# Performance work log

Measured on AMD Instinct MI355X. Metric: run time of the kernel, lower is better.

The kernel has to match this reference:

```python
import jax, jax.numpy as jnp
import numpy as np

T = 2048; HIDDEN = 2048; HQ = 32; G = 2; D = 64
KERNEL = 32; STRIDE = 16; BLOCK = 64; TOPK = 16
INIT_BLOCKS = 1; LOCAL_BLOCKS = 2; WINDOW = 512
ROPE_BASE = 10000.0
NEG = -1e30


def _rope(x):
    # x: [T, H, D], non-interleaved rotate-half rope
    t, h, d = x.shape
    half = d // 2
    inv = 1.0 / (ROPE_BASE ** (jnp.arange(half, dtype=jnp.float32) / half))
    freqs = jnp.arange(t, dtype=jnp.float32)[:, None] * inv[None, :]
    cos = jnp.cos(freqs)[:, None, :]
    sin = jnp.sin(freqs)[:, None, :]
    x1, x2 = x[..., :half], x[..., half:]
    return jnp.concatenate([x1 * cos - x2 * sin, x2 * cos + x1 * sin], axis=-1)


def setup_inputs() -> dict:
    key = jax.random.key(0)
    ks = jax.random.split(key, 8)
    s = 0.02
    return {
        "hidden_states": jax.random.normal(ks[0], (1, T, HIDDEN), jnp.float32),
        "Wq": jax.random.normal(ks[1], (HQ * D, HIDDEN), jnp.float32) * s,
        "Wk": jax.random.normal(ks[2], (G * D, HIDDEN), jnp.float32) * s,
        "Wv": jax.random.normal(ks[3], (G * D, HIDDEN), jnp.float32) * s,
        "Wo": jax.random.normal(ks[4], (HIDDEN, HQ * D), jnp.float32) * s,
        "Wgate": jax.random.normal(ks[5], (3, HIDDEN), jnp.float32) * s,
        "compress_key": jax.random.normal(ks[6], (G, D * KERNEL, D), jnp.float32) * s,
        "compress_value": jax.random.normal(ks[7], (G, D * KERNEL, D), jnp.float32) * s,
    }


def reference(hidden_states, Wq, Wk, Wv, Wo, Wgate, compress_key, compress_value):
    x = hidden_states[0]                      # [T, HIDDEN] (single varlen sequence)
    scale = 1.0 / np.sqrt(D).astype(np.float32)
    q = (x @ Wq.T).reshape(T, HQ, D)
    k = (x @ Wk.T).reshape(T, G, D)
    v = (x @ Wv.T).reshape(T, G, D)
    gate = jax.nn.sigmoid(x @ Wgate.T)        # [T, 3]
    q = _rope(q)
    k = _rope(k)

    # --- branch 1: compressed attention (linear_compress + compressed_attention) ---
    C = (T - KERNEL) // STRIDE + 1            # compressed sequence length
    starts = jnp.arange(C) * STRIDE
    win_idx = starts[:, None] + jnp.arange(KERNEL)[None, :]        # [C, KERNEL]
    kw = k[win_idx].transpose(2, 0, 1, 3).reshape(G, C, KERNEL * D)
    vw = v[win_idx].transpose(2, 0, 1, 3).reshape(G, C, KERNEL * D)
    ck = jnp.einsum('gcf,gfd->cgd', kw, compress_key)              # [C, G, D]
    cv = jnp.einsum('gcf,gfd->cgd', vw, compress_value)

    qg = q.reshape(T, G, HQ // G, D)          # [T, G, group, D]
    cs = jnp.einsum('tghd,cgd->ghtc', qg, ck) * scale              # [G, grp, T, C]
    # query i may attend compressed token j iff i >= j*stride + kernel - 1
    cmask = jnp.arange(T)[:, None] >= (starts + KERNEL - 1)[None, :]  # [T, C]
    cs = jnp.where(cmask[None, None], cs, NEG)
    p = jax.nn.softmax(cs, axis=-1)
    valid = cmask.any(-1)                     # queries with >=1 compressed key
    p = jnp.where(valid[None, None, :, None], p, 0.0)
    comp_out = jnp.einsum('ghtc,cgd->tghd', p, cv).reshape(T, HQ, D)

    # --- topk block selection from pooled compressed attention scores ---
    NB = T // BLOCK
    bstart = jnp.arange(NB) * BLOCK
    # compressed token j overlaps key block b
    overlap = ((starts[:, None] < bstart[None, :] + BLOCK) &
               (starts[:, None] + KERNEL > bstart[None, :])).astype(p.dtype)  # [C, NB]
    score = jnp.einsum('ghtc,cb->gtb', p, overlap)                 # [G, T, NB]
    qblock = jnp.arange(T) // BLOCK
    b = jnp.arange(NB)
    causal_b = b[None, :] <= qblock[:, None]                       # [T, NB]
    forced = (b[None, :] < INIT_BLOCKS) | (((qblock[:, None] - b[None, :]) < LOCAL_BLOCKS) & causal_b)
    score = jnp.where(forced[None], jnp.inf, score)
    score = jnp.where(causal_b[None], score, -jnp.inf)
    _, topk_idx = jax.lax.top_k(score, TOPK)                       # [G, T, TOPK]
    tk_valid = jnp.take_along_axis(score, topk_idx, axis=-1) > -jnp.inf
    sel = ((topk_idx[..., None] == b) & tk_valid[..., None]).any(axis=2)  # [G, T, NB]

    # --- branch 2: topk block-sparse attention ---
    key_block = jnp.arange(T) // BLOCK
    keymask = sel[:, :, key_block]                                 # [G, T, Tk]
    causal = jnp.arange(T)[:, None] >= jnp.arange(T)[None, :]      # [T, Tk]
    smask = keymask & causal[None]
    ss = jnp.einsum('tghd,sgd->ghts', qg, k) * scale               # [G, grp, T, Tk]
    ss = jnp.where(smask[:, None], ss, NEG)
    sparse_out = jnp.einsum('ghts,sgd->tghd', jax.nn.softmax(ss, -1), v).reshape(T, HQ, D)

    # --- branch 3: sliding window attention (causal, left window) ---
    delta = jnp.arange(T)[:, None] - jnp.arange(T)[None, :]
    wmask = (delta >= 0) & (delta <= WINDOW)                       # [T, Tk]
    ws = jnp.einsum('tghd,sgd->ghts', qg, k) * scale
    ws = jnp.where(wmask[None, None], ws, NEG)
    slide_out = jnp.einsum('ghts,sgd->tghd', jax.nn.softmax(ws, -1), v).reshape(T, HQ, D)

    # --- learned gate fusion + output projection ---
    out = (gate[:, 0, None, None] * comp_out +
           gate[:, 1, None, None] * sparse_out +
           gate[:, 2, None, None] * slide_out)                    # [T, HQ, D]
    o = out.reshape(T, HQ * D) @ Wo.T
    return o[None]                                                 # [1, T, HIDDEN]
```

## Files before the change

kernel.cpp:

```cpp
#include <hip/hip_runtime.h>
#include <math.h>

#define T_SEQ 2048
#define NHQ 32
#define NG 2
#define HD 64
#define CSTRIDE 16
#define KVGW 384

#if defined(__has_builtin)
#if __has_builtin(__builtin_amdgcn_exp2f)
#define EXP2(x) __builtin_amdgcn_exp2f(x)
#endif
#endif
#ifndef EXP2
#define EXP2(x) __expf(0.6931471805599453f * (x))
#endif

typedef __attribute__((ext_vector_type(8))) short short8_t;
typedef __attribute__((ext_vector_type(4))) short short4_t;
typedef __attribute__((ext_vector_type(4))) float f32x4;

__device__ __forceinline__ ushort f2bf(float x) {
  union { float f; unsigned u; } c; c.f = x;
  unsigned r = c.u + 0x7fff + ((c.u >> 16) & 1);
  return (ushort)(r >> 16);
}
__device__ __forceinline__ float bf2f(ushort u) {
  union { unsigned u; float f; } c; c.u = ((unsigned)u) << 16;
  return c.f;
}

__device__ __forceinline__ void glds16(const ushort* g, ushort* l) {
  __builtin_amdgcn_global_load_lds(
      (const __attribute__((address_space(1))) unsigned int*)g,
      (__attribute__((address_space(3))) unsigned int*)l, 16, 0, 0);
}

__global__ __launch_bounds__(256) void mgemm(
    const ushort* __restrict__ A, const ushort* __restrict__ B,
    float* __restrict__ C, int M, int N, int K) {
  __shared__ __align__(16) ushort As[128 * 64];
  __shared__ __align__(16) ushort Bs[64 * 64];
  const int tid = threadIdx.x;
  const int lane = tid & 63, w = tid >> 6;
  const int quad = lane >> 4, l16 = lane & 15;
  const int m0 = blockIdx.y * 128, n0 = blockIdx.x * 64;
  const int mq = (w & 1) * 64, nq = (w >> 1) * 32;
  f32x4 acc[4][2];
  const f32x4 fz = {0.f, 0.f, 0.f, 0.f};
  #pragma unroll
  for (int i = 0; i < 4; ++i)
    #pragma unroll
    for (int j = 0; j < 2; ++j) acc[i][j] = fz;

  for (int k0 = 0; k0 < K; k0 += 64) {
    __syncthreads();
    #pragma unroll
    for (int j = 0; j < 4; ++j) {
      int ci = j * 256 + tid;
      int row = ci >> 3, cl = ci & 7;
      int kc = cl ^ (row & 7);
      glds16(A + ((size_t)(m0 + row) * K + k0 + kc * 8), &As[ci * 8]);
    }
    #pragma unroll
    for (int j = 0; j < 2; ++j) {
      int ci = j * 256 + tid;
      int row = ci >> 3, cl = ci & 7;
      int kc = cl ^ (row & 7);
      glds16(B + ((size_t)(n0 + row) * K + k0 + kc * 8), &Bs[ci * 8]);
    }
    __syncthreads();
    #pragma unroll
    for (int kt = 0; kt < 2; ++kt) {
      short8_t af[4], bf_[2];
      #pragma unroll
      for (int mt = 0; mt < 4; ++mt) {
        int row = mq + mt * 16 + l16;
        int cl = (kt * 4 + quad) ^ (row & 7);
        af[mt] = *(const short8_t*)&As[row * 64 + cl * 8];
      }
      #pragma unroll
      for (int nt = 0; nt < 2; ++nt) {
        int row = nq + nt * 16 + l16;
        int cl = (kt * 4 + quad) ^ (row & 7);
        bf_[nt] = *(const short8_t*)&Bs[row * 64 + cl * 8];
      }
      #pragma unroll
      for (int mt = 0; mt < 4; ++mt)
        #pragma unroll
        for (int nt = 0; nt < 2; ++nt)
          acc[mt][nt] = __builtin_amdgcn_mfma_f32_16x16x32_bf16(
              af[mt], bf_[nt], acc[mt][nt], 0, 0, 0);
    }
  }
  #pragma unroll
  for (int mt = 0; mt < 4; ++mt)
    #pragma unroll
    for (int nt = 0; nt < 2; ++nt)
      #pragma unroll
      for (int r = 0; r < 4; ++r) {
        int m = m0 + mq + mt * 16 + quad * 4 + r;
        int n = n0 + nq + nt * 16 + l16;
        C[(size_t)m * N + n] = acc[mt][nt][r];
      }
}

__global__ __launch_bounds__(256) void cvt_bf(const float* __restrict__ src,
                                              ushort* __restrict__ dst, int n) {
  int i = (blockIdx.x * 256 + threadIdx.x) * 4;
  if (i >= n) return;
  float4 v = *(const float4*)(src + i);
  short4_t o = {(short)f2bf(v.x), (short)f2bf(v.y),
                (short)f2bf(v.z), (short)f2bf(v.w)};
  *(short4_t*)(dst + i) = o;
}

__global__ __launch_bounds__(256) void pack_wkvg(
    const float* __restrict__ Wk, const float* __restrict__ Wv,
    const float* __restrict__ Wg, ushort* __restrict__ dst) {
  int i = blockIdx.x * 256 + threadIdx.x;
  if (i >= KVGW * 2048) return;
  int n = i >> 11, k = i & 2047;
  float v;
  if (n < 128) v = Wk[(size_t)n * 2048 + k];
  else if (n < 256) v = Wv[(size_t)(n - 128) * 2048 + k];
  else if (n < 259) v = Wg[(size_t)(n - 256) * 2048 + k];
  else v = 0.f;
  dst[i] = f2bf(v);
}

__global__ __launch_bounds__(256) void cvt_vt(const float* __restrict__ kvg,
                                              ushort* __restrict__ vt) {
  int i = blockIdx.x * 256 + threadIdx.x;
  if (i >= T_SEQ * NG * HD) return;
  int d = i & 63, g = (i >> 6) & 1, s = i >> 7;
  int blk = s >> 6, k = s & 63;
  int snew = blk * 64 + (((k >> 2) ^ (d & 15)) << 2) + (k & 3);
  vt[((size_t)g * HD + d) * T_SEQ + snew] =
      f2bf(kvg[(size_t)s * KVGW + 128 + g * 64 + d]);
}

__global__ __launch_bounds__(256) void rope_all(
    const float* __restrict__ q, float* __restrict__ kvg,
    ushort* __restrict__ qbf, ushort* __restrict__ kbf) {
  const int t = blockIdx.x;
  const float lnb_over = 9.210340371976184f / 32.f;
  const float QS = 0.18033688011112042f;
  for (int job = threadIdx.x; job < (NHQ + NG) * 32; job += 256) {
    int h = job >> 5, j = job & 31;
    float inv = expf(-(float)j * lnb_over);
    float fr = (float)t * inv;
    float c_ = cosf(fr), s_ = sinf(fr);
    if (h < NHQ) {
      const float cq = c_ * QS, sq = s_ * QS;
      const float* base = q + ((size_t)t * NHQ + h) * HD;
      float x1 = base[j], x2 = base[j + 32];
      ushort* ob = qbf + ((size_t)t * NHQ + h) * HD;
      ob[j] = f2bf(x1 * cq - x2 * sq);
      ob[j + 32] = f2bf(x2 * cq + x1 * sq);
    } else {
      int g = h - NHQ;
      float* base = kvg + (size_t)t * KVGW + g * 64;
      float x1 = base[j], x2 = base[j + 32];
      float o1 = x1 * c_ - x2 * s_, o2 = x2 * c_ + x1 * s_;
      base[j] = o1; base[j + 32] = o2;
      kbf[(size_t)t * 128 + g * 64 + j] = f2bf(o1);
      kbf[(size_t)t * 128 + g * 64 + j + 32] = f2bf(o2);
    }
  }
}

__global__ __launch_bounds__(256) void compress_kv(
    const float* __restrict__ kvg,
    const float* __restrict__ Wck, const float* __restrict__ Wcv,
    ushort* __restrict__ ck16, ushort* __restrict__ cvt16) {
  const int c = blockIdx.x, g = blockIdx.y;
  const int tid = threadIdx.x;
  if (c == 127) {
    if (tid < 64) ck16[((size_t)127 * NG + g) * HD + tid] = 0;
    else if (tid < 128) cvt16[((size_t)g * HD + (tid - 64)) * 128 + 127] = 0;
    return;
  }
  const int d = tid & 63, chunk = tid >> 6;
  __shared__ float red[2][4][64];
  float ak = 0.f, av = 0.f;
  #pragma unroll 4
  for (int f = chunk * 512; f < chunk * 512 + 512; ++f) {
    int i = f >> 6, e = f & 63;
    int trow = c * CSTRIDE + i;
    float kv = kvg[(size_t)trow * KVGW + g * 64 + e];
    float vv = kvg[(size_t)trow * KVGW + 128 + g * 64 + e];
    ak += kv * Wck[((size_t)g * 2048 + f) * HD + d];
    av += vv * Wcv[((size_t)g * 2048 + f) * HD + d];
  }
  red[0][chunk][d] = ak;
  red[1][chunk][d] = av;
  __syncthreads();
  if (tid < 64) {
    ck16[((size_t)c * NG + g) * HD + tid] =
        f2bf(red[0][0][tid] + red[0][1][tid] + red[0][2][tid] + red[0][3][tid]);
  } else if (tid < 128) {
    int dd = tid - 64;
    cvt16[((size_t)g * HD + dd) * 128 + c] =
        f2bf(red[1][0][dd] + red[1][1][dd] + red[1][2][dd] + red[1][3][dd]);
  }
}

__global__ __launch_bounds__(512) void comp_attn(
    const ushort* __restrict__ qbf, const ushort* __restrict__ ck16,
    const ushort* __restrict__ cvt16, const float* __restrict__ kvg,
    float* __restrict__ comb, unsigned* __restrict__ sel) {
  const int tb = 127 - blockIdx.x, g = blockIdx.y;
  const int t0 = tb * 16;
  const int tid = threadIdx.x, lane = tid & 63, w = tid >> 6;
  const int quad = lane >> 4, l16 = lane & 15;
  const int qb = t0 >> 6;

  __shared__ float colsum[16][129];
  for (int i = tid; i < 16 * 129; i += 512) ((float*)colsum)[i] = 0.f;
  __syncthreads();

  const int t = t0 + l16;
  const int cmaxv = (t >= 31) ? min(126, (t - 31) >> 4) : -1;
  const int h0 = w * 2;

  short8_t qB[2][2];
  #pragma unroll
  for (int hh = 0; hh < 2; ++hh)
    #pragma unroll
    for (int kd = 0; kd < 2; ++kd)
      qB[hh][kd] = *(const short8_t*)(qbf +
          ((size_t)t * NHQ + g * 16 + h0 + hh) * HD + kd * 32 + quad * 8);

  const f32x4 fz = {0.f, 0.f, 0.f, 0.f};
  f32x4 sp[2][8];

  #pragma unroll
  for (int ct = 0; ct < 8; ++ct) {
    const ushort* kr = ck16 + ((size_t)(ct * 16 + l16) * NG + g) * HD + quad * 8;
    short8_t kA0 = *(const short8_t*)kr;
    short8_t kA1 = *(const short8_t*)(kr + 32);
    #pragma unroll
    for (int hh = 0; hh < 2; ++hh) {
      f32x4 c0 = __builtin_amdgcn_mfma_f32_16x16x32_bf16(kA0, qB[hh][0], fz, 0, 0, 0);
      sp[hh][ct] = __builtin_amdgcn_mfma_f32_16x16x32_bf16(kA1, qB[hh][1], c0, 0, 0, 0);
    }
  }

  short4_t pB[2][8];
  #pragma unroll
  for (int hh = 0; hh < 2; ++hh) {
    float mx = -INFINITY;
    #pragma unroll
    for (int ct = 0; ct < 8; ++ct)
      #pragma unroll
      for (int r = 0; r < 4; ++r) {
        int c = ct * 16 + quad * 4 + r;
        float s_ = (c <= cmaxv) ? sp[hh][ct][r] : -INFINITY;
        sp[hh][ct][r] = s_;
        mx = fmaxf(mx, s_);
      }
    mx = fmaxf(mx, __shfl_xor(mx, 16));
    mx = fmaxf(mx, __shfl_xor(mx, 32));
    if (mx == -INFINITY) mx = 0.f;
    float ls = 0.f;
    #pragma unroll
    for (int ct = 0; ct < 8; ++ct)
      #pragma unroll
      for (int r = 0; r < 4; ++r) {
        float p = EXP2(sp[hh][ct][r] - mx);
        sp[hh][ct][r] = p;
        ls += p;
      }
    ls += __shfl_xor(ls, 16);
    ls += __shfl_xor(ls, 32);
    float inv = (ls > 0.f) ? 1.f / ls : 0.f;
    #pragma unroll
    for (int ct = 0; ct < 8; ++ct) {
      short4_t pk;
      #pragma unroll
      for (int r = 0; r < 4; ++r) {
        float pn = sp[hh][ct][r] * inv;
        sp[hh][ct][r] = pn;
        pk[r] = (short)f2bf(pn);
      }
      pB[hh][ct] = pk;
    }
  }

  #pragma unroll
  for (int ct = 0; ct < 8; ++ct)
    #pragma unroll
    for (int r = 0; r < 4; ++r)
      atomicAdd(&colsum[l16][ct * 16 + quad * 4 + r],
                sp[0][ct][r] + sp[1][ct][r]);

  f32x4 acc[2][4];
  #pragma unroll
  for (int hh = 0; hh < 2; ++hh)
    #pragma unroll
    for (int dt = 0; dt < 4; ++dt) acc[hh][dt] = fz;
  #pragma unroll
  for (int ct = 0; ct < 8; ++ct) {
    short4_t vA[4];
    #pragma unroll
    for (int dt = 0; dt < 4; ++dt)
      vA[dt] = *(const short4_t*)(cvt16 +
          ((size_t)g * HD + dt * 16 + l16) * 128 + ct * 16 + quad * 4);
    #pragma unroll
    for (int hh = 0; hh < 2; ++hh)
      #pragma unroll
      for (int dt = 0; dt < 4; ++dt)
        acc[hh][dt] = __builtin_amdgcn_mfma_f32_16x16x16bf16_1k(
            vA[dt], pB[hh][ct], acc[hh][dt], 0, 0, 0);
  }

  const float g0 = 1.f / (1.f + __expf(-kvg[(size_t)t * KVGW + 256]));
  #pragma unroll
  for (int hh = 0; hh < 2; ++hh)
    #pragma unroll
    for (int dt = 0; dt < 4; ++dt)
      #pragma unroll
      for (int r = 0; r < 4; ++r)
        comb[((size_t)t * NHQ + g * 16 + h0 + hh) * HD + dt * 16 + quad * 4 + r] =
            g0 * acc[hh][dt][r];

  __syncthreads();

  {
    const int tl = tid >> 5;
    const int b = tid & 31;
    float s;
    if (b > qb) s = -INFINITY;
    else if (b == 0 || qb - b < 2) s = INFINITY;
    else {
      s = 0.f;
      #pragma unroll
      for (int i = 0; i < 5; ++i) s += colsum[tl][4 * b - 1 + i];
    }
    unsigned key = (s < 0.f) ? 0u : (__float_as_uint(s) + 1u);
    unsigned msel = 0;
    for (int it = 0; it < 16; ++it) {
      unsigned long long pk =
          (((unsigned long long)key) << 6) | (unsigned)(63 - b);
      #pragma unroll
      for (int off = 16; off >= 1; off >>= 1) {
        unsigned long long o = __shfl_xor(pk, off);
        if (o > pk) pk = o;
      }
      if ((pk >> 6) == 0) break;
      int bs = 63 - (int)(pk & 63);
      msel |= 1u << bs;
      if (b == bs) key = 0;
    }
    if (b == 0) sel[(size_t)(t0 + tl) * NG + g] = msel;
  }
}

__global__ __launch_bounds__(512, 2) void mfma_attn(
    const ushort* __restrict__ qb16, const ushort* __restrict__ kb16,
    const ushort* __restrict__ vtb, const float* __restrict__ kvg,
    const unsigned* __restrict__ sel, const float* __restrict__ comb1,
    ushort* __restrict__ combb) {
  const int g = blockIdx.y;
  const int hgp = blockIdx.z;
  const int qb = (hgp >= 4) ? blockIdx.x : 31 - blockIdx.x;
  const int tid = threadIdx.x, lane = tid & 63, w = tid >> 6;
  const int quad = lane >> 4, l16 = lane & 15;
  const int head = g * 16 + hgp * 2 + (w >> 2);
  const int t0 = qb * 64;

  __shared__ __align__(16) ushort Ks[2][64 * 64];
  __shared__ __align__(16) ushort Vs[2][64 * 64];
  __shared__ unsigned sel_s[64];

  if (tid < 64) sel_s[tid] = sel[(size_t)(t0 + tid) * NG + g];
  __syncthreads();

  const int qg = t0 + (w & 3) * 16 + l16;
  const unsigned sbq = sel_s[(w & 3) * 16 + l16];

  short8_t qB0 = *(const short8_t*)(qb16 +
      ((size_t)qg * NHQ + head) * HD + quad * 8);
  short8_t qB1 = *(const short8_t*)(qb16 +
      ((size_t)qg * NHQ + head) * HD + 32 + quad * 8);

  float m0 = -1e30f, m1 = -1e30f;
  f32x4 acc0[4], acc1[4], accL0, accL1;
  const f32x4 fz = {0.f, 0.f, 0.f, 0.f};
  #pragma unroll
  for (int dt = 0; dt < 4; ++dt) { acc0[dt] = fz; acc1[dt] = fz; }
  accL0 = fz; accL1 = fz;
  const short4_t onesA = {(short)0x3F80, (short)0x3F80,
                          (short)0x3F80, (short)0x3F80};

  unsigned uni = sel_s[lane];
  #pragma unroll
  for (int off = 32; off >= 1; off >>= 1) uni |= __shfl_xor(uni, off);
  const int b0w = (qb > 8) ? qb - 8 : 0;
  const unsigned wmask = ((1u << (qb - b0w + 1)) - 1u) << b0w;
  unsigned lrem = uni | wmask;
  const int nb = __popc(lrem);

  #define STAGE(buf, blk)                                                     \
    {                                                                         \
      const int blk_ = (blk);                                                 \
      const int row = tid >> 3, cl = tid & 7;                                 \
      const int kck = cl ^ (row & 7);                                         \
      glds16(kb16 + (size_t)(blk_ * 64 + row) * 128 + g * 64 + kck * 8,       \
             &Ks[buf][tid * 8]);                                              \
      glds16(vtb + ((size_t)g * 64 + row) * 2048 + blk_ * 64 + cl * 8,        \
             &Vs[buf][tid * 8]);                                              \
    }

  int blkcur = __ffs(lrem) - 1; lrem &= lrem - 1;
  STAGE(0, blkcur);
  __syncthreads();

  const int e = l16 & 7;

  for (int ib = 0; ib < nb; ++ib) {
    const int cur = ib & 1;
    const int blk = blkcur;
    if (ib + 1 < nb) {
      blkcur = __ffs(lrem) - 1; lrem &= lrem - 1;
      STAGE(cur ^ 1, blkcur);
    }

    f32x4 sp[4];
    __builtin_amdgcn_s_setprio(1);
    #pragma unroll
    for (int kt = 0; kt < 4; ++kt) {
      const ushort* kr = &Ks[cur][(kt * 16 + l16) * 64];
      short8_t kA0 = *(const short8_t*)(kr + ((quad ^ e) * 8));
      short8_t kA1 = *(const short8_t*)(kr + ((quad ^ e ^ 4) * 8));
      f32x4 c = __builtin_amdgcn_mfma_f32_16x16x32_bf16(kA0, qB0, fz, 0, 0, 0);
      sp[kt] = __builtin_amdgcn_mfma_f32_16x16x32_bf16(kA1, qB1, c, 0, 0, 0);
    }
    __builtin_amdgcn_s_setprio(0);

    const bool diag = (blk == qb);
    const bool wedge = (blk == qb - 8);
    const bool inU = ((uni >> blk) & 1u) != 0;
    const bool inW = ((wmask >> blk) & 1u) != 0;
    const bool selq = ((sbq >> blk) & 1u) != 0;

    float rm = -INFINITY;
    #pragma unroll
    for (int kt = 0; kt < 4; ++kt)
      #pragma unroll
      for (int r = 0; r < 4; ++r) rm = fmaxf(rm, sp[kt][r]);
    rm = fmaxf(rm, __shfl_xor(rm, 16));
    rm = fmaxf(rm, __shfl_xor(rm, 32));

    if (inU && __any(selq)) {
      float mx;
      if (!diag) {
        mx = selq ? rm : -INFINITY;
      } else {
        mx = -INFINITY;
        #pragma unroll
        for (int kt = 0; kt < 4; ++kt)
          #pragma unroll
          for (int r = 0; r < 4; ++r) {
            int key = blk * 64 + kt * 16 + quad * 4 + r;
            bool ok = selq && (key <= qg);
            mx = ok ? fmaxf(mx, sp[kt][r]) : mx;
          }
        mx = fmaxf(mx, __shfl_xor(mx, 16));
        mx = fmaxf(mx, __shfl_xor(mx, 32));
      }
      if (!__all(mx <= m0 + 11.f)) {
        float mnew = fmaxf(m0, mx);
        float alpha = EXP2(m0 - mnew);
        #pragma unroll
        for (int dt = 0; dt < 4; ++dt)
          #pragma unroll
          for (int r = 0; r < 4; ++r) acc0[dt][r] *= alpha;
        #pragma unroll
        for (int r = 0; r < 4; ++r) accL0[r] *= alpha;
        m0 = mnew;
      }
      short4_t pB[4];
      #pragma unroll
      for (int kt = 0; kt < 4; ++kt) {
        union { unsigned u[2]; short4_t s; } pk;
        if (!diag) {
          float p0 = EXP2(sp[kt][0] - m0), p1 = EXP2(sp[kt][1] - m0);
          float p2 = EXP2(sp[kt][2] - m0), p3 = EXP2(sp[kt][3] - m0);
          asm("v_cvt_pk_bf16_f32 %0, %1, %2" : "=v"(pk.u[0]) : "v"(p0), "v"(p1));
          asm("v_cvt_pk_bf16_f32 %0, %1, %2" : "=v"(pk.u[1]) : "v"(p2), "v"(p3));
          pk.u[0] = selq ? pk.u[0] : 0u;
          pk.u[1] = selq ? pk.u[1] : 0u;
        } else {
          float p[4];
          #pragma unroll
          for (int r = 0; r < 4; ++r) {
            int key = blk * 64 + kt * 16 + quad * 4 + r;
            bool ok = selq && (key <= qg);
            p[r] = ok ? EXP2(sp[kt][r] - m0) : 0.f;
          }
          asm("v_cvt_pk_bf16_f32 %0, %1, %2" : "=v"(pk.u[0]) : "v"(p[0]), "v"(p[1]));
          asm("v_cvt_pk_bf16_f32 %0, %1, %2" : "=v"(pk.u[1]) : "v"(p[2]), "v"(p[3]));
        }
        pB[kt] = pk.s;
      }
      __builtin_amdgcn_s_setprio(1);
      #pragma unroll
      for (int kt = 0; kt < 4; ++kt) {
        #pragma unroll
        for (int dt = 0; dt < 4; ++dt) {
          short4_t vA = *(const short4_t*)(&Vs[cur][(dt * 16 + l16) * 64 +
                                                    (((kt * 4 + quad) ^ l16) << 2)]);
          acc0[dt] = __builtin_amdgcn_mfma_f32_16x16x16bf16_1k(
              vA, pB[kt], acc0[dt], 0, 0, 0);
        }
        accL0 = __builtin_amdgcn_mfma_f32_16x16x16bf16_1k(
            onesA, pB[kt], accL0, 0, 0, 0);
      }
      __builtin_amdgcn_s_setprio(0);
    }

    if (inW) {
      float mx;
      if (!diag && !wedge) {
        mx = rm;
      } else {
        mx = -INFINITY;
        #pragma unroll
        for (int kt = 0; kt < 4; ++kt)
          #pragma unroll
          for (int r = 0; r < 4; ++r) {
            int key = blk * 64 + kt * 16 + quad * 4 + r;
            bool ok = (key <= qg) && (qg - key <= 512);
            mx = ok ? fmaxf(mx, sp[kt][r]) : mx;
          }
        mx = fmaxf(mx, __shfl_xor(mx, 16));
        mx = fmaxf(mx, __shfl_xor(mx, 32));
      }
      if (!__all(mx <= m1 + 11.f)) {
        float mnew = fmaxf(m1, mx);
        float alpha = EXP2(m1 - mnew);
        #pragma unroll
        for (int dt = 0; dt < 4; ++dt)
          #pragma unroll
          for (int r = 0; r < 4; ++r) acc1[dt][r] *= alpha;
        #pragma unroll
        for (int r = 0; r < 4; ++r) accL1[r] *= alpha;
        m1 = mnew;
      }
      short4_t pB[4];
      #pragma unroll
      for (int kt = 0; kt < 4; ++kt) {
        union { unsigned u[2]; short4_t s; } pk;
        if (!diag && !wedge) {
          float p0 = EXP2(sp[kt][0] - m1), p1 = EXP2(sp[kt][1] - m1);
          float p2 = EXP2(sp[kt][2] - m1), p3 = EXP2(sp[kt][3] - m1);
          asm("v_cvt_pk_bf16_f32 %0, %1, %2" : "=v"(pk.u[0]) : "v"(p0), "v"(p1));
          asm("v_cvt_pk_bf16_f32 %0, %1, %2" : "=v"(pk.u[1]) : "v"(p2), "v"(p3));
        } else {
          float p[4];
          #pragma unroll
          for (int r = 0; r < 4; ++r) {
            int key = blk * 64 + kt * 16 + quad * 4 + r;
            bool ok = (key <= qg) && (qg - key <= 512);
            p[r] = ok ? EXP2(sp[kt][r] - m1) : 0.f;
          }
          asm("v_cvt_pk_bf16_f32 %0, %1, %2" : "=v"(pk.u[0]) : "v"(p[0]), "v"(p[1]));
          asm("v_cvt_pk_bf16_f32 %0, %1, %2" : "=v"(pk.u[1]) : "v"(p[2]), "v"(p[3]));
        }
        pB[kt] = pk.s;
      }
      __builtin_amdgcn_s_setprio(1);
      #pragma unroll
      for (int kt = 0; kt < 4; ++kt) {
        #pragma unroll
        for (int dt = 0; dt < 4; ++dt) {
          short4_t vA = *(const short4_t*)(&Vs[cur][(dt * 16 + l16) * 64 +
                                                    (((kt * 4 + quad) ^ l16) << 2)]);
          acc1[dt] = __builtin_amdgcn_mfma_f32_16x16x16bf16_1k(
              vA, pB[kt], acc1[dt], 0, 0, 0);
        }
        accL1 = __builtin_amdgcn_mfma_f32_16x16x16bf16_1k(
            onesA, pB[kt], accL1, 0, 0, 0);
      }
      __builtin_amdgcn_s_setprio(0);
    }

    __syncthreads();
  }
  #undef STAGE

  const float c0 =
      (1.f / (1.f + __expf(-kvg[(size_t)qg * KVGW + 257]))) / accL0[0];
  const float c1 =
      (1.f / (1.f + __expf(-kvg[(size_t)qg * KVGW + 258]))) / accL1[0];
  #pragma unroll
  for (int dt = 0; dt < 4; ++dt) {
    const size_t base = ((size_t)qg * NHQ + head) * HD + dt * 16 + quad * 4;
    f32x4 cv = *(const f32x4*)(comb1 + base);
    short4_t o;
    #pragma unroll
    for (int r = 0; r < 4; ++r)
      o[r] = (short)f2bf(cv[r] + c0 * acc0[dt][r] + c1 * acc1[dt][r]);
    *(short4_t*)(combb + base) = o;
  }
}

extern "C" void kernel_launch(void* const* d_in, const int* in_sizes, int n_in,
                              void* d_out, int out_size, void* d_ws, size_t ws_size,
                              hipStream_t stream) {
  const float* x   = (const float*)d_in[0];
  const float* Wq  = (const float*)d_in[1];
  const float* Wk  = (const float*)d_in[2];
  const float* Wv  = (const float*)d_in[3];
  const float* Wo  = (const float*)d_in[4];
  const float* Wg  = (const float*)d_in[5];
  const float* Wck = (const float*)d_in[6];
  const float* Wcv = (const float*)d_in[7];
  float* out = (float*)d_out;
  float* ws = (float*)d_ws;

  float* qbuf   = ws;
  float* comb1  = qbuf + 4194304;
  float* kvg    = comb1 + 4194304;
  float* ckb    = kvg + 786432;
  float* cvb    = ckb + 16384;
  unsigned* sel = (unsigned*)(cvb + 16384);
  ushort* kbf   = (ushort*)(sel + 4096);
  ushort* vtb   = kbf + 262144;
  ushort* wkvgb = vtb + 262144;
  ushort* regA  = wkvgb + 786432;
  ushort* regB  = regA + 4194304;
  ushort* xb = regA;      ushort* combb = regA;
  ushort* wqb = regB;     ushort* qbf = regB;
  ushort* wob = (ushort*)qbuf;

  ushort* ckb16 = (ushort*)ckb;
  ushort* cvtb  = ckb16 + 16384;

  const int CV4 = (1048576 + 255) / 256;
  cvt_bf<<<CV4, 256, 0, stream>>>(x, xb, 4194304);
  cvt_bf<<<CV4, 256, 0, stream>>>(Wq, wqb, 4194304);
  pack_wkvg<<<(KVGW * 2048 + 255) / 256, 256, 0, stream>>>(Wk, Wv, Wg, wkvgb);

  mgemm<<<dim3(32, 16), 256, 0, stream>>>(xb, wqb, qbuf, 2048, 2048, 2048);
  mgemm<<<dim3(6, 16), 256, 0, stream>>>(xb, wkvgb, kvg, 2048, KVGW, 2048);

  rope_all<<<2048, 256, 0, stream>>>(qbuf, kvg, qbf, kbf);
  cvt_bf<<<CV4, 256, 0, stream>>>(Wo, wob, 4194304);
  cvt_vt<<<(262144 + 255) / 256, 256, 0, stream>>>(kvg, vtb);
  compress_kv<<<dim3(128, 2), 256, 0, stream>>>(kvg, Wck, Wcv, ckb16, cvtb);
  comp_attn<<<dim3(128, 2), 512, 0, stream>>>(qbf, ckb16, cvtb, kvg, comb1, sel);
  mfma_attn<<<dim3(32, 2, 8), 512, 0, stream>>>(qbf, kbf, vtb, kvg, sel, comb1, combb);

  mgemm<<<dim3(32, 16), 256, 0, stream>>>(combb, wob, out, 2048, 2048, 2048);
}
```

Before: 354.7 us.

## Split-K the KV/gate projection GEMM and skip masked compressed tiles

The small KV/gate projection GEMM (96 blocks) is split four ways along K into a new mgemm_ks kernel, with a sum4 kernel reducing the partials. This puts more blocks on the GPU for an otherwise underfilled launch. The comp_attn kernel also skips whole 16-column compressed-key tiles that lie entirely beyond the causal limit, removing wasted MFMA, exp and atomic work for early query blocks. The cost is extra partial-sum traffic and one more launch. The partials reuse the comb1 buffer as scratch.

After: 352.6 us. About the same (-0.6%).

```diff
diff --git a/kernel.cpp b/kernel.cpp
--- a/kernel.cpp
+++ b/kernel.cpp
@@ -104,6 +104,91 @@
         int n = n0 + nq + nt * 16 + l16;
         C[(size_t)m * N + n] = acc[mt][nt][r];
       }
+}
+
+__global__ __launch_bounds__(256) void mgemm_ks(
+    const ushort* __restrict__ A, const ushort* __restrict__ B,
+    float* __restrict__ Cp, int M, int N, int K) {
+  __shared__ __align__(16) ushort As[128 * 64];
+  __shared__ __align__(16) ushort Bs[64 * 64];
+  const int tid = threadIdx.x;
+  const int lane = tid & 63, w = tid >> 6;
+  const int quad = lane >> 4, l16 = lane & 15;
+  const int m0 = blockIdx.y * 128, n0 = blockIdx.x * 64;
+  const int mq = (w & 1) * 64, nq = (w >> 1) * 32;
+  const int kq = K >> 2;
+  const int kbeg = blockIdx.z * kq, kend = kbeg + kq;
+  float* C = Cp + (size_t)blockIdx.z * M * N;
+  f32x4 acc[4][2];
+  const f32x4 fz = {0.f, 0.f, 0.f, 0.f};
+  #pragma unroll
+  for (int i = 0; i < 4; ++i)
+    #pragma unroll
+    for (int j = 0; j < 2; ++j) acc[i][j] = fz;
+
+  for (int k0 = kbeg; k0 < kend; k0 += 64) {
+    __syncthreads();
+    #pragma unroll
+    for (int j = 0; j < 4; ++j) {
+      int ci = j * 256 + tid;
+      int row = ci >> 3, cl = ci & 7;
+      int kc = cl ^ (row & 7);
+      glds16(A + ((size_t)(m0 + row) * K + k0 + kc * 8), &As[ci * 8]);
+    }
+    #pragma unroll
+    for (int j = 0; j < 2; ++j) {
+      int ci = j * 256 + tid;
+      int row = ci >> 3, cl = ci & 7;
+      int kc = cl ^ (row & 7);
+      glds16(B + ((size_t)(n0 + row) * K + k0 + kc * 8), &Bs[ci * 8]);
+    }
+    __syncthreads();
+    #pragma unroll
+    for (int kt = 0; kt < 2; ++kt) {
+      short8_t af[4], bf_[2];
+      #pragma unroll
+      for (int mt = 0; mt < 4; ++mt) {
+        int row = mq + mt * 16 + l16;
+        int cl = (kt * 4 + quad) ^ (row & 7);
+        af[mt] = *(const short8_t*)&As[row * 64 + cl * 8];
+      }
+      #pragma unroll
+      for (int nt = 0; nt < 2; ++nt) {
+        int row = nq + nt * 16 + l16;
+        int cl = (kt * 4 + quad) ^ (row & 7);
+        bf_[nt] = *(const short8_t*)&Bs[row * 64 + cl * 8];
+      }
+      #pragma unroll
+      for (int mt = 0; mt < 4; ++mt)
+        #pragma unroll
+        for (int nt = 0; nt < 2; ++nt)
+          acc[mt][nt] = __builtin_amdgcn_mfma_f32_16x16x32_bf16(
+              af[mt], bf_[nt], acc[mt][nt], 0, 0, 0);
+    }
+  }
+  #pragma unroll
+  for (int mt = 0; mt < 4; ++mt)
+    #pragma unroll
+    for (int nt = 0; nt < 2; ++nt)
+      #pragma unroll
+      for (int r = 0; r < 4; ++r) {
+        int m = m0 + mq + mt * 16 + quad * 4 + r;
+        int n = n0 + nq + nt * 16 + l16;
+        C[(size_t)m * N + n] = acc[mt][nt][r];
+      }
+}
+
+__global__ __launch_bounds__(256) void sum4(const float* __restrict__ p,
+                                            float* __restrict__ dst, int n) {
+  int i = (blockIdx.x * 256 + threadIdx.x) * 4;
+  if (i >= n) return;
+  float4 a = *(const float4*)(p + i);
+  float4 b = *(const float4*)(p + n + i);
+  float4 c = *(const float4*)(p + 2 * (size_t)n + i);
+  float4 d = *(const float4*)(p + 3 * (size_t)n + i);
+  float4 o = {a.x + b.x + c.x + d.x, a.y + b.y + c.y + d.y,
+              a.z + b.z + c.z + d.z, a.w + b.w + c.w + d.w};
+  *(float4*)(dst + i) = o;
 }
 
 __global__ __launch_bounds__(256) void cvt_bf(const float* __restrict__ src,
@@ -216,6 +301,7 @@
   const int tid = threadIdx.x, lane = tid & 63, w = tid >> 6;
   const int quad = lane >> 4, l16 = lane & 15;
   const int qb = t0 >> 6;
+  const int ctmax = (t0 >= 16) ? ((t0 - 16) >> 8) : -1;
 
   __shared__ float colsum[16][129];
   for (int i = tid; i < 16 * 129; i += 512) ((float*)colsum)[i] = 0.f;
@@ -238,13 +324,15 @@
 
   #pragma unroll
   for (int ct = 0; ct < 8; ++ct) {
-    const ushort* kr = ck16 + ((size_t)(ct * 16 + l16) * NG + g) * HD + quad * 8;
-    short8_t kA0 = *(const short8_t*)kr;
-    short8_t kA1 = *(const short8_t*)(kr + 32);
-    #pragma unroll
-    for (int hh = 0; hh < 2; ++hh) {
-      f32x4 c0 = __builtin_amdgcn_mfma_f32_16x16x32_bf16(kA0, qB[hh][0], fz, 0, 0, 0);
-      sp[hh][ct] = __builtin_amdgcn_mfma_f32_16x16x32_bf16(kA1, qB[hh][1], c0, 0, 0, 0);
+    if (ct <= ctmax) {
+      const ushort* kr = ck16 + ((size_t)(ct * 16 + l16) * NG + g) * HD + quad * 8;
+      short8_t kA0 = *(const short8_t*)kr;
+      short8_t kA1 = *(const short8_t*)(kr + 32);
+      #pragma unroll
+      for (int hh = 0; hh < 2; ++hh) {
+        f32x4 c0 = __builtin_amdgcn_mfma_f32_16x16x32_bf16(kA0, qB[hh][0], fz, 0, 0, 0);
+        sp[hh][ct] = __builtin_amdgcn_mfma_f32_16x16x32_bf16(kA1, qB[hh][1], c0, 0, 0, 0);
+      }
     }
   }
 
@@ -253,48 +341,59 @@
   for (int hh = 0; hh < 2; ++hh) {
     float mx = -INFINITY;
     #pragma unroll
-    for (int ct = 0; ct < 8; ++ct)
-      #pragma unroll
-      for (int r = 0; r < 4; ++r) {
-        int c = ct * 16 + quad * 4 + r;
-        float s_ = (c <= cmaxv) ? sp[hh][ct][r] : -INFINITY;
-        sp[hh][ct][r] = s_;
-        mx = fmaxf(mx, s_);
-      }
+    for (int ct = 0; ct < 8; ++ct) {
+      if (ct <= ctmax) {
+        #pragma unroll
+        for (int r = 0; r < 4; ++r) {
+          int c = ct * 16 + quad * 4 + r;
+          float s_ = (c <= cmaxv) ? sp[hh][ct][r] : -INFINITY;
+          sp[hh][ct][r] = s_;
+          mx = fmaxf(mx, s_);
+        }
+      }
+    }
     mx = fmaxf(mx, __shfl_xor(mx, 16));
     mx = fmaxf(mx, __shfl_xor(mx, 32));
     if (mx == -INFINITY) mx = 0.f;
     float ls = 0.f;
     #pragma unroll
-    for (int ct = 0; ct < 8; ++ct)
-      #pragma unroll
-      for (int r = 0; r < 4; ++r) {
-        float p = EXP2(sp[hh][ct][r] - mx);
-        sp[hh][ct][r] = p;
-        ls += p;
-      }
+    for (int ct = 0; ct < 8; ++ct) {
+      if (ct <= ctmax) {
+        #pragma unroll
+        for (int r = 0; r < 4; ++r) {
+          float p = EXP2(sp[hh][ct][r] - mx);
+          sp[hh][ct][r] = p;
+          ls += p;
+        }
+      }
+    }
     ls += __shfl_xor(ls, 16);
     ls += __shfl_xor(ls, 32);
     float inv = (ls > 0.f) ? 1.f / ls : 0.f;
     #pragma unroll
     for (int ct = 0; ct < 8; ++ct) {
-      short4_t pk;
-      #pragma unroll
-      for (int r = 0; r < 4; ++r) {
-        float pn = sp[hh][ct][r] * inv;
-        sp[hh][ct][r] = pn;
-        pk[r] = (short)f2bf(pn);
-      }
-      pB[hh][ct] = pk;
-    }
-  }
-
-  #pragma unroll
-  for (int ct = 0; ct < 8; ++ct)
-    #pragma unroll
-    for (int r = 0; r < 4; ++r)
-      atomicAdd(&colsum[l16][ct * 16 + quad * 4 + r],
-                sp[0][ct][r] + sp[1][ct][r]);
+      if (ct <= ctmax) {
+        short4_t pk;
+        #pragma unroll
+        for (int r = 0; r < 4; ++r) {
+          float pn = sp[hh][ct][r] * inv;
+          sp[hh][ct][r] = pn;
+          pk[r] = (short)f2bf(pn);
+        }
+        pB[hh][ct] = pk;
+      }
+    }
+  }
+
+  #pragma unroll
+  for (int ct = 0; ct < 8; ++ct) {
+    if (ct <= ctmax) {
+      #pragma unroll
+      for (int r = 0; r < 4; ++r)
+        atomicAdd(&colsum[l16][ct * 16 + quad * 4 + r],
+                  sp[0][ct][r] + sp[1][ct][r]);
+    }
+  }
 
   f32x4 acc[2][4];
   #pragma unroll
@@ -303,17 +402,19 @@
     for (int dt = 0; dt < 4; ++dt) acc[hh][dt] = fz;
   #pragma unroll
   for (int ct = 0; ct < 8; ++ct) {
-    short4_t vA[4];
-    #pragma unroll
-    for (int dt = 0; dt < 4; ++dt)
-      vA[dt] = *(const short4_t*)(cvt16 +
-          ((size_t)g * HD + dt * 16 + l16) * 128 + ct * 16 + quad * 4);
-    #pragma unroll
-    for (int hh = 0; hh < 2; ++hh)
+    if (ct <= ctmax) {
+      short4_t vA[4];
       #pragma unroll
       for (int dt = 0; dt < 4; ++dt)
-        acc[hh][dt] = __builtin_amdgcn_mfma_f32_16x16x16bf16_1k(
-            vA[dt], pB[hh][ct], acc[hh][dt], 0, 0, 0);
+        vA[dt] = *(const short4_t*)(cvt16 +
+            ((size_t)g * HD + dt * 16 + l16) * 128 + ct * 16 + quad * 4);
+      #pragma unroll
+      for (int hh = 0; hh < 2; ++hh)
+        #pragma unroll
+        for (int dt = 0; dt < 4; ++dt)
+          acc[hh][dt] = __builtin_amdgcn_mfma_f32_16x16x16bf16_1k(
+              vA[dt], pB[hh][ct], acc[hh][dt], 0, 0, 0);
+    }
   }
 
   const float g0 = 1.f / (1.f + __expf(-kvg[(size_t)t * KVGW + 256]));
@@ -646,7 +747,8 @@
   pack_wkvg<<<(KVGW * 2048 + 255) / 256, 256, 0, stream>>>(Wk, Wv, Wg, wkvgb);
 
   mgemm<<<dim3(32, 16), 256, 0, stream>>>(xb, wqb, qbuf, 2048, 2048, 2048);
-  mgemm<<<dim3(6, 16), 256, 0, stream>>>(xb, wkvgb, kvg, 2048, KVGW, 2048);
+  mgemm_ks<<<dim3(6, 16, 4), 256, 0, stream>>>(xb, wkvgb, comb1, 2048, KVGW, 2048);
+  sum4<<<(786432 / 4 + 255) / 256, 256, 0, stream>>>(comb1, kvg, 786432);
 
   rope_all<<<2048, 256, 0, stream>>>(qbuf, kvg, qbf, kbf);
   cvt_bf<<<CV4, 256, 0, stream>>>(Wo, wob, 4194304);
```
